# Performance work log

Measured on AMD Instinct MI355X. Metric: run time of the kernel, lower is better.

The kernel has to match this reference:

```python
import jax, jax.numpy as jnp
import numpy as np

B, S, D, E, K = 4, 2048, 1024, 8, 2


def setup_inputs() -> dict:
    key = jax.random.key(0)
    k1, k2, k3 = jax.random.split(key, 3)
    scale = 1.0 / np.sqrt(D)
    x = jax.random.normal(k1, (B, S, D), dtype=jnp.float32)
    Wg = jax.random.normal(k2, (D, E), dtype=jnp.float32) * scale
    bg = jnp.zeros((E,), dtype=jnp.float32)
    We = jax.random.normal(k3, (E, D, D), dtype=jnp.float32) * scale
    be = jnp.zeros((E, D), dtype=jnp.float32)
    return {"x": x, "Wg": Wg, "bg": bg, "We": We, "be": be}


def reference(x, Wg, bg, We, be):
    # gate scores: [B, S, E]
    gate_scores = jnp.einsum("bsd,de->bse", x, Wg) + bg
    topk_values, topk_indices = jax.lax.top_k(gate_scores, K)
    # mask: -inf everywhere except at top-k indices (where value == score)
    sel = jax.nn.one_hot(topk_indices, E, dtype=jnp.bool_).any(axis=-2)  # [B,S,E]
    masked = jnp.where(sel, gate_scores, -jnp.inf)
    gate_weights = jax.nn.softmax(masked, axis=-1)  # [B,S,E]
    # dense all-expert compute, as in the original: [B,S,E,D]
    expert_outputs = jnp.einsum("bsd,edh->bseh", x, We) + be
    fused = jnp.einsum("bse,bseh->bsh", gate_weights, expert_outputs)
    return fused
```

## Files before the change

kernel.cpp:

```cpp
#include <hip/hip_runtime.h>
#include <stdint.h>

#define NTOK   8192
#define DIM    1024
#define NEXP   8
#define MAXP   8192

#define BM 128
#define BN 128
#define BK 32

typedef float  f32x4  __attribute__((ext_vector_type(4)));
typedef __bf16 bf16x8 __attribute__((ext_vector_type(8)));

typedef __attribute__((address_space(1))) const void* gas_ptr;
typedef __attribute__((address_space(3))) void*       las_ptr;

__device__ __forceinline__ unsigned short f32_to_bf16(float f) {
  union { float f; unsigned int u; } v; v.f = f;
  unsigned int u = v.u;
  unsigned int r = (u + 0x7FFFu + ((u >> 16) & 1u)) >> 16;
  return (unsigned short)r;
}

__global__ __launch_bounds__(256) void transpose_we(
    const float* __restrict__ We, unsigned short* __restrict__ Wt) {
  __shared__ float tile[64][65];
  const int e  = blockIdx.z;
  const int d0 = blockIdx.y * 64;
  const int h0 = blockIdx.x * 64;
  const int t  = threadIdx.x;
  const int tx = t & 63, ty = t >> 6;
  const float* src = We + (size_t)e * DIM * DIM;
#pragma unroll
  for (int i = 0; i < 16; ++i) {
    int d = ty + i * 4;
    tile[d][tx] = src[(size_t)(d0 + d) * DIM + (h0 + tx)];
  }
  __syncthreads();
  unsigned short* dst = Wt + (size_t)e * DIM * DIM;
  const int tx2 = t & 31, ty8 = t >> 5;
#pragma unroll
  for (int i = 0; i < 8; ++i) {
    int h = ty8 + i * 8;
    int d = tx2 * 2;
    unsigned int pk = (unsigned int)f32_to_bf16(tile[d][h]) |
                      ((unsigned int)f32_to_bf16(tile[d + 1][h]) << 16);
    *(unsigned int*)&dst[(size_t)(h0 + h) * DIM + d0 + d] = pk;
  }
}

__global__ __launch_bounds__(256) void gate_score(
    const float* __restrict__ x, const float* __restrict__ Wg,
    const float* __restrict__ bg, unsigned short* __restrict__ Xbf,
    int* __restrict__ tok_ee, float2* __restrict__ tok_w) {
  const int wave = threadIdx.x >> 6;
  const int lane = threadIdx.x & 63;
  const int tok  = blockIdx.x * 4 + wave;

  const float* xr = x + (size_t)tok * DIM + lane * 16;
  float xs[16];
#pragma unroll
  for (int i = 0; i < 4; ++i) *(f32x4*)&xs[i * 4] = *(const f32x4*)(xr + i * 4);

  unsigned int packed[8];
#pragma unroll
  for (int i = 0; i < 8; ++i)
    packed[i] = (unsigned int)f32_to_bf16(xs[2 * i]) |
                ((unsigned int)f32_to_bf16(xs[2 * i + 1]) << 16);
  uint4* xb = (uint4*)(Xbf + (size_t)tok * DIM + lane * 16);
  xb[0] = make_uint4(packed[0], packed[1], packed[2], packed[3]);
  xb[1] = make_uint4(packed[4], packed[5], packed[6], packed[7]);

  double acc[8] = {0, 0, 0, 0, 0, 0, 0, 0};
  const float* wr = Wg + (size_t)(lane * 16) * NEXP;
#pragma unroll
  for (int i = 0; i < 16; ++i) {
    f32x4 wa = *(const f32x4*)(wr + i * 8);
    f32x4 wb = *(const f32x4*)(wr + i * 8 + 4);
    double xd = (double)xs[i];
    acc[0] += xd * (double)wa[0]; acc[1] += xd * (double)wa[1];
    acc[2] += xd * (double)wa[2]; acc[3] += xd * (double)wa[3];
    acc[4] += xd * (double)wb[0]; acc[5] += xd * (double)wb[1];
    acc[6] += xd * (double)wb[2]; acc[7] += xd * (double)wb[3];
  }
#pragma unroll
  for (int m = 1; m < 64; m <<= 1) {
#pragma unroll
    for (int e = 0; e < 8; ++e) acc[e] += __shfl_xor(acc[e], m, 64);
  }

  if (lane == 0) {
    float s[8];
#pragma unroll
    for (int e = 0; e < 8; ++e) s[e] = (float)acc[e] + bg[e];
    int i0 = 0; float v0 = s[0];
#pragma unroll
    for (int e = 1; e < 8; ++e) if (s[e] > v0) { v0 = s[e]; i0 = e; }
    int i1 = -1; float v1 = -3.4e38f;
#pragma unroll
    for (int e = 0; e < 8; ++e) if (e != i0 && s[e] > v1) { v1 = s[e]; i1 = e; }
    float t1 = expf(v1 - v0);
    float den = 1.0f + t1;
    tok_ee[tok] = i0 | (i1 << 8);
    tok_w[tok]  = make_float2(1.0f / den, t1 / den);
  }
}

__global__ __launch_bounds__(1024) void compact_kernel(
    const int* __restrict__ tok_ee, const float2* __restrict__ tok_w,
    int* __restrict__ counts, int* __restrict__ pair_token,
    float* __restrict__ pair_w) {
  __shared__ int wave_cnt[16][NEXP];
  __shared__ int wave_off[16][NEXP];
  __shared__ int base[NEXP];
  __shared__ int chunk_tot[NEXP];
  const int tid = threadIdx.x, wave = tid >> 6, lane = tid & 63;
  if (tid < NEXP) base[tid] = 0;
  __syncthreads();
  for (int c = 0; c < NTOK / 1024; ++c) {
    const int t = c * 1024 + tid;
    const int p = tok_ee[t];
    const int e0 = p & 255, e1 = (p >> 8) & 255;
    const float2 w = tok_w[t];
    int pre0 = 0, pre1 = 0;
    const unsigned long long below = (1ull << lane) - 1ull;
#pragma unroll
    for (int e = 0; e < NEXP; ++e) {
      unsigned long long m = __ballot(e0 == e || e1 == e);
      if (e0 == e) pre0 = __popcll(m & below);
      if (e1 == e) pre1 = __popcll(m & below);
      if (lane == 0) wave_cnt[wave][e] = __popcll(m);
    }
    __syncthreads();
    if (tid < NEXP) {
      int s = 0;
      for (int w2 = 0; w2 < 16; ++w2) {
        wave_off[w2][tid] = s;
        s += wave_cnt[w2][tid];
      }
      chunk_tot[tid] = s;
    }
    __syncthreads();
    const int s0 = base[e0] + wave_off[wave][e0] + pre0;
    const int s1 = base[e1] + wave_off[wave][e1] + pre1;
    pair_token[e0 * MAXP + s0] = (t << 1);     pair_w[e0 * MAXP + s0] = w.x;
    pair_token[e1 * MAXP + s1] = (t << 1) | 1; pair_w[e1 * MAXP + s1] = w.y;
    __syncthreads();
    if (tid < NEXP) base[tid] += chunk_tot[tid];
    __syncthreads();
  }
  if (tid < NEXP) counts[tid] = base[tid];
}

__global__ __launch_bounds__(256) void moe_gemm(
    const unsigned short* __restrict__ Xbf, const unsigned short* __restrict__ Wt,
    const float* __restrict__ be, const int* __restrict__ counts,
    const int* __restrict__ pair_token, const float* __restrict__ pair_w,
    float* __restrict__ part, float* __restrict__ Y, int use_part) {
  const int e   = blockIdx.z;
  const int cnt = counts[e];
  const int m0  = blockIdx.y * BM;
  if (m0 >= cnt) return;
  const int n0  = blockIdx.x * BN;

  __shared__ __align__(16) unsigned short As[2][BM * BK];
  __shared__ __align__(16) unsigned short Bs[2][BN * BK];

  const int tid  = threadIdx.x;
  const int wave = tid >> 6;
  const int lane = tid & 63;
  const int fm   = lane & 15;
  const int fq   = lane >> 4;
  const int wm   = wave >> 1;
  const int wn   = wave & 1;

  const int srow = wave * 32 + (lane >> 2);
  const int kc   = (lane & 3) * 8;
  const unsigned short* gA[2];
  const unsigned short* gB[2];
#pragma unroll
  for (int c = 0; c < 2; ++c) {
    int r  = srow + c * 16;
    int gr = m0 + r;
    int tk = (gr < cnt) ? (pair_token[e * MAXP + gr] >> 1) : 0;
    gA[c] = Xbf + (size_t)tk * DIM + kc;
    gB[c] = Wt + (size_t)e * DIM * DIM + (size_t)(n0 + r) * DIM + kc;
  }

#define STAGE(buf, koff)                                                      \
  {                                                                           \
    _Pragma("unroll") for (int c = 0; c < 2; ++c) {                           \
      __builtin_amdgcn_global_load_lds(                                       \
          (gas_ptr)(uintptr_t)(gA[c] + (koff)),                               \
          (las_ptr)(uintptr_t)(&As[buf][(wave * 2 + c) * 512]), 16, 0, 0);    \
      __builtin_amdgcn_global_load_lds(                                       \
          (gas_ptr)(uintptr_t)(gB[c] + (koff)),                               \
          (las_ptr)(uintptr_t)(&Bs[buf][(wave * 2 + c) * 512]), 16, 0, 0);    \
    }                                                                         \
  }

  f32x4 acc[4][4];
#pragma unroll
  for (int i = 0; i < 4; ++i)
#pragma unroll
    for (int j = 0; j < 4; ++j) { f32x4 z = {0.f, 0.f, 0.f, 0.f}; acc[i][j] = z; }

  STAGE(0, 0);
  int cur = 0;
  for (int k0 = 0; k0 < DIM; k0 += BK) {
    __syncthreads();
    if (k0 + BK < DIM) STAGE(cur ^ 1, k0 + BK);

    bf16x8 af[4], bfr[4];
#pragma unroll
    for (int i = 0; i < 4; ++i)
      af[i] = *(const bf16x8*)&As[cur][(wm * 64 + i * 16 + fm) * BK + fq * 8];
#pragma unroll
    for (int j = 0; j < 4; ++j)
      bfr[j] = *(const bf16x8*)&Bs[cur][(wn * 64 + j * 16 + fm) * BK + fq * 8];
#pragma unroll
    for (int i = 0; i < 4; ++i)
#pragma unroll
      for (int j = 0; j < 4; ++j)
        acc[i][j] = __builtin_amdgcn_mfma_f32_16x16x32_bf16(af[i], bfr[j],
                                                            acc[i][j], 0, 0, 0);
    cur ^= 1;
  }
#undef STAGE

  int   rowv[4][4];
  float wrow[4][4];
#pragma unroll
  for (int i = 0; i < 4; ++i)
#pragma unroll
    for (int r = 0; r < 4; ++r) {
      int gr = m0 + wm * 64 + i * 16 + fq * 4 + r;
      bool valid = gr < cnt;
      rowv[i][r] = valid ? pair_token[e * MAXP + gr] : -1;
      wrow[i][r] = valid ? pair_w[e * MAXP + gr] : 0.f;
    }
  if (use_part) {
#pragma unroll
    for (int j = 0; j < 4; ++j) {
      int col = n0 + wn * 64 + j * 16 + fm;
      float bev = be[e * DIM + col];
#pragma unroll
      for (int i = 0; i < 4; ++i)
#pragma unroll
        for (int r = 0; r < 4; ++r) {
          int v = rowv[i][r];
          if (v >= 0)
            part[(size_t)v * DIM + col] = wrow[i][r] * (acc[i][j][r] + bev);
        }
    }
  } else {
#pragma unroll
    for (int j = 0; j < 4; ++j) {
      int col = n0 + wn * 64 + j * 16 + fm;
      float bev = be[e * DIM + col];
#pragma unroll
      for (int i = 0; i < 4; ++i)
#pragma unroll
        for (int r = 0; r < 4; ++r) {
          int v = rowv[i][r];
          if (v >= 0)
            atomicAdd(Y + (size_t)(v >> 1) * DIM + col,
                      wrow[i][r] * (acc[i][j][r] + bev));
        }
    }
  }
}

__global__ __launch_bounds__(256) void reduce_pairs(
    const float* __restrict__ part, float* __restrict__ Y) {
  const int g = blockIdx.x * 256 + threadIdx.x;
  const int t = g >> 8;
  const int o = (g & 255) * 4;
  const f32x4 a = *(const f32x4*)(part + (size_t)(2 * t) * DIM + o);
  const f32x4 b = *(const f32x4*)(part + (size_t)(2 * t + 1) * DIM + o);
  *(f32x4*)(Y + (size_t)t * DIM + o) = a + b;
}

extern "C" void kernel_launch(void* const* d_in, const int* in_sizes, int n_in,
                              void* d_out, int out_size, void* d_ws, size_t ws_size,
                              hipStream_t stream) {
  const float* x  = (const float*)d_in[0];
  const float* Wg = (const float*)d_in[1];
  const float* bg = (const float*)d_in[2];
  const float* We = (const float*)d_in[3];
  const float* be = (const float*)d_in[4];
  float* Y = (float*)d_out;

  const size_t MB = 1024 * 1024;
  char* ws = (char*)d_ws;
  unsigned short* Xbf = (unsigned short*)ws;
  unsigned short* Wt  = (unsigned short*)(ws + 16 * MB);
  const size_t part_bytes = (size_t)NTOK * 2 * DIM * 4;
  const size_t need = 32 * MB + part_bytes + 1 * MB;
  const int use_part = ws_size >= need;
  float* part = (float*)(ws + 32 * MB);
  char* p2 = ws + 32 * MB + (use_part ? part_bytes : 0);
  int*    counts     = (int*)p2;
  int*    pair_token = (int*)(p2 + 256);
  float*  pair_w     = (float*)(p2 + 256 + 262144);
  int*    tok_ee     = (int*)(p2 + 256 + 2 * 262144);
  float2* tok_w      = (float2*)(p2 + 256 + 2 * 262144 + 32768);

  if (!use_part)
    hipMemsetAsync(d_out, 0, (size_t)out_size * sizeof(float), stream);

  transpose_we<<<dim3(16, 16, NEXP), 256, 0, stream>>>(We, Wt);
  gate_score<<<NTOK / 4, 256, 0, stream>>>(x, Wg, bg, Xbf, tok_ee, tok_w);
  compact_kernel<<<1, 1024, 0, stream>>>(tok_ee, tok_w, counts, pair_token,
                                         pair_w);
  moe_gemm<<<dim3(8, NTOK / BM, NEXP), 256, 0, stream>>>(
      Xbf, Wt, be, counts, pair_token, pair_w, part, Y, use_part);
  if (use_part)
    reduce_pairs<<<NTOK * DIM / 4 / 256, 256, 0, stream>>>(part, Y);
}
```

Measured before the change: 254.7 us.

## Load MFMA fragments directly from global memory, dropping LDS staging

The MoE GEMM no longer stages A and B tiles through double-buffered shared memory via global_load_lds. Each lane now loads its bf16x8 MFMA fragments straight from global memory into registers, with a register double buffer and a fully unrolled K loop, so no barriers remain. This removes LDS traffic and the per-iteration __syncthreads. The cost is that each wave fetches its fragments independently, so the block's waves load overlapping rows redundantly and rely on L2/L1 for reuse. The 16-byte loads per lane stride across rows and coalesce poorly, and register pressure goes up.

```diff
diff --git a/kernel.cpp b/kernel.cpp
--- a/kernel.cpp
+++ b/kernel.cpp
@@ -8,13 +8,9 @@
 
 #define BM 128
 #define BN 128
-#define BK 32
 
 typedef float  f32x4  __attribute__((ext_vector_type(4)));
 typedef __bf16 bf16x8 __attribute__((ext_vector_type(8)));
-
-typedef __attribute__((address_space(1))) const void* gas_ptr;
-typedef __attribute__((address_space(3))) void*       las_ptr;
 
 __device__ __forceinline__ unsigned short f32_to_bf16(float f) {
   union { float f; unsigned int u; } v; v.f = f;
@@ -164,9 +160,6 @@
   if (m0 >= cnt) return;
   const int n0  = blockIdx.x * BN;
 
-  __shared__ __align__(16) unsigned short As[2][BM * BK];
-  __shared__ __align__(16) unsigned short Bs[2][BN * BK];
-
   const int tid  = threadIdx.x;
   const int wave = tid >> 6;
   const int lane = tid & 63;
@@ -175,29 +168,18 @@
   const int wm   = wave >> 1;
   const int wn   = wave & 1;
 
-  const int srow = wave * 32 + (lane >> 2);
-  const int kc   = (lane & 3) * 8;
-  const unsigned short* gA[2];
-  const unsigned short* gB[2];
-#pragma unroll
-  for (int c = 0; c < 2; ++c) {
-    int r  = srow + c * 16;
-    int gr = m0 + r;
+  const unsigned short* pA[4];
+  const unsigned short* pB[4];
+#pragma unroll
+  for (int i = 0; i < 4; ++i) {
+    int gr = m0 + wm * 64 + i * 16 + fm;
     int tk = (gr < cnt) ? (pair_token[e * MAXP + gr] >> 1) : 0;
-    gA[c] = Xbf + (size_t)tk * DIM + kc;
-    gB[c] = Wt + (size_t)e * DIM * DIM + (size_t)(n0 + r) * DIM + kc;
-  }
-
-#define STAGE(buf, koff)                                                      \
-  {                                                                           \
-    _Pragma("unroll") for (int c = 0; c < 2; ++c) {                           \
-      __builtin_amdgcn_global_load_lds(                                       \
-          (gas_ptr)(uintptr_t)(gA[c] + (koff)),                               \
-          (las_ptr)(uintptr_t)(&As[buf][(wave * 2 + c) * 512]), 16, 0, 0);    \
-      __builtin_amdgcn_global_load_lds(                                       \
-          (gas_ptr)(uintptr_t)(gB[c] + (koff)),                               \
-          (las_ptr)(uintptr_t)(&Bs[buf][(wave * 2 + c) * 512]), 16, 0, 0);    \
-    }                                                                         \
+    pA[i] = Xbf + (size_t)tk * DIM + fq * 8;
+  }
+#pragma unroll
+  for (int j = 0; j < 4; ++j) {
+    int nr = n0 + wn * 64 + j * 16 + fm;
+    pB[j] = Wt + (size_t)e * DIM * DIM + (size_t)nr * DIM + fq * 8;
   }
 
   f32x4 acc[4][4];
@@ -206,28 +188,30 @@
 #pragma unroll
     for (int j = 0; j < 4; ++j) { f32x4 z = {0.f, 0.f, 0.f, 0.f}; acc[i][j] = z; }
 
-  STAGE(0, 0);
-  int cur = 0;
-  for (int k0 = 0; k0 < DIM; k0 += BK) {
-    __syncthreads();
-    if (k0 + BK < DIM) STAGE(cur ^ 1, k0 + BK);
-
-    bf16x8 af[4], bfr[4];
+  bf16x8 af[2][4], bfr[2][4];
+#pragma unroll
+  for (int i = 0; i < 4; ++i) af[0][i] = *(const bf16x8*)(pA[i]);
+#pragma unroll
+  for (int j = 0; j < 4; ++j) bfr[0][j] = *(const bf16x8*)(pB[j]);
+
+#pragma unroll
+  for (int s = 0; s < DIM / 32; ++s) {
+    const int cur = s & 1, nxt = cur ^ 1;
+    if (s + 1 < DIM / 32) {
+      const int ko = (s + 1) * 32;
+#pragma unroll
+      for (int i = 0; i < 4; ++i) af[nxt][i] = *(const bf16x8*)(pA[i] + ko);
+#pragma unroll
+      for (int j = 0; j < 4; ++j) bfr[nxt][j] = *(const bf16x8*)(pB[j] + ko);
+    }
 #pragma unroll
     for (int i = 0; i < 4; ++i)
-      af[i] = *(const bf16x8*)&As[cur][(wm * 64 + i * 16 + fm) * BK + fq * 8];
-#pragma unroll
-    for (int j = 0; j < 4; ++j)
-      bfr[j] = *(const bf16x8*)&Bs[cur][(wn * 64 + j * 16 + fm) * BK + fq * 8];
-#pragma unroll
-    for (int i = 0; i < 4; ++i)
 #pragma unroll
       for (int j = 0; j < 4; ++j)
-        acc[i][j] = __builtin_amdgcn_mfma_f32_16x16x32_bf16(af[i], bfr[j],
+        acc[i][j] = __builtin_amdgcn_mfma_f32_16x16x32_bf16(af[cur][i],
+                                                            bfr[cur][j],
                                                             acc[i][j], 0, 0, 0);
-    cur ^= 1;
-  }
-#undef STAGE
+  }
 
   int   rowv[4][4];
   float wrow[4][4];
```

New measurement: 365.1 us. 1.43x slower.
